# Optimization experiments

Hardware: AMD Instinct MI355X
Metric: run time of the kernel (lower is better)

The kernel has to match this reference:

```python
import jax, jax.numpy as jnp
import numpy as np

N = 100_000   # number of sparse points
C = 128       # channels
K3 = 27       # 3x3x3 kernel offsets


def sparse_conv(x, nbr, W, b):
    """Minkowski-style sparse conv: gather-GEMM-scatter.
    x:   [N, Cin] point features
    nbr: [N, K3] neighbor index per kernel offset; index N -> missing (zero row)
    W:   [K3, Cin, Cout], b: [Cout]
    """
    x_pad = jnp.concatenate([x, jnp.zeros((1, x.shape[1]), x.dtype)], axis=0)

    def step(acc, wk_nk):
        Wk, nk = wk_nk                      # Wk: [Cin,Cout], nk: [N]
        return acc + x_pad[nk] @ Wk, None   # gather + GEMM, accumulate

    acc0 = jnp.broadcast_to(b, (x.shape[0], W.shape[2])).astype(x.dtype)
    acc, _ = jax.lax.scan(step, acc0, (W, nbr.T))
    return acc


def setup_inputs() -> dict:
    key = jax.random.key(0)
    ks = jax.random.split(key, 12)
    Ch = C // 2

    def w(k, shape, fan_in):
        return jax.random.normal(k, shape, dtype=jnp.float32) / np.sqrt(fan_in)

    x = jax.random.normal(ks[0], (N, C), dtype=jnp.float32)
    # neighbor map; value N means "no neighbor" (maps to zero-padded row)
    nbr = jax.random.randint(ks[1], (N, K3), 0, N + 1, dtype=jnp.int32)

    return {
        "x": x,
        "nbr": nbr,
        "W00": w(ks[2], (K3, C, Ch), K3 * C),   # conv0_0: kxkxk, C -> C/2
        "b00": jnp.zeros((Ch,), jnp.float32),
        "W01": w(ks[3], (K3, Ch, Ch), K3 * Ch),  # conv0_1: kxkxk, C/2 -> C/2
        "b01": jnp.zeros((Ch,), jnp.float32),
        "W10": w(ks[4], (C, Ch), C),             # conv1_0: 1x1x1, C -> C/2
        "b10": jnp.zeros((Ch,), jnp.float32),
        "W11": w(ks[5], (K3, Ch, Ch), K3 * Ch),  # conv1_1: kxkxk, C/2 -> C/2
        "b11": jnp.zeros((Ch,), jnp.float32),
        "W12": w(ks[6], (Ch, Ch), Ch),           # conv1_2: 1x1x1, C/2 -> C/2
        "b12": jnp.zeros((Ch,), jnp.float32),
    }


def reference(x, nbr, W00, b00, W01, b01, W10, b10, W11, b11, W12, b12):
    # branch 0: conv -> relu -> conv
    h0 = jax.nn.relu(sparse_conv(x, nbr, W00, b00))
    out0 = sparse_conv(h0, nbr, W01, b01)
    # branch 1: 1x1 conv -> relu -> conv -> relu -> 1x1 conv
    h1 = jax.nn.relu(x @ W10 + b10)
    h1 = jax.nn.relu(sparse_conv(h1, nbr, W11, b11))
    out1 = h1 @ W12 + b12
    # concat channels, residual add
    return jnp.concatenate([out0, out1], axis=1) + x
```

## Files before the change

kernel.cpp:

```cpp
#include <hip/hip_runtime.h>
#include <hip/hip_bf16.h>
#include <stdint.h>

typedef __bf16 bf16x8 __attribute__((ext_vector_type(8)));
typedef float  f32x4  __attribute__((ext_vector_type(4)));

#define MFMA(A, B, C) __builtin_amdgcn_mfma_f32_16x16x32_bf16((A), (B), (C), 0, 0, 0)

#define LDS_BARRIER() asm volatile("s_waitcnt lgkmcnt(0)\n\ts_barrier" ::: "memory")

static __device__ __forceinline__ unsigned short f2b(float f) {
    union { float f; unsigned int u; } v; v.f = f;
    return (unsigned short)((v.u + 0x7FFFu + ((v.u >> 16) & 1u)) >> 16);
}

static __device__ __forceinline__ bf16x8 perm_frag(int sel, bf16x8 D) {
    union { bf16x8 v; int d[4]; } u, r;
    u.v = D;
#pragma unroll
    for (int w = 0; w < 4; ++w) r.d[w] = __builtin_amdgcn_ds_bpermute(sel, u.d[w]);
    return r.v;
}

__global__ __launch_bounds__(256) void convert_kernel(
    const float* __restrict__ x, unsigned short* __restrict__ xb,
    unsigned short* __restrict__ hb, int N) {
    long long i = (long long)blockIdx.x * blockDim.x + threadIdx.x;
    long long base = i * 4;
    long long nx = (long long)N * 128;
    long long total = nx + 128;
    if (base >= total) return;
    if (base < nx) {
        float4 v = *(const float4*)(x + base);
        ushort4 o;
        o.x = f2b(v.x); o.y = f2b(v.y); o.z = f2b(v.z); o.w = f2b(v.w);
        *(ushort4*)(xb + base) = o;
    } else {
        ushort4 z = make_ushort4(0, 0, 0, 0);
        *(ushort4*)(xb + base) = z;
        *(ushort4*)(hb + base) = z;
    }
}

__global__ __launch_bounds__(256) void pack_kernel(
    const float* __restrict__ W00, const float* __restrict__ W01,
    const float* __restrict__ W10, const float* __restrict__ W11,
    const float* __restrict__ W12,
    unsigned short* __restrict__ wp00, unsigned short* __restrict__ wpC,
    unsigned short* __restrict__ wp10, unsigned short* __restrict__ wp12) {
    int g = blockIdx.x * blockDim.x + threadIdx.x;
    const float* W; int cinSteps; int which;
    if (g < 27648)      { W = W00; cinSteps = 4; which = 0; }
    else if (g < 41472) { g -= 27648; W = W01; cinSteps = 2; which = 1; }
    else if (g < 55296) { g -= 41472; W = W11; cinSteps = 2; which = 2; }
    else if (g < 56320) { g -= 55296; W = W10; cinSteps = 4; which = 3; }
    else if (g < 56832) { g -= 56320; W = W12; cinSteps = 2; which = 4; }
    else return;
    int lane = g & 63;
    int st   = g >> 6;
    int t    = st & 3;
    int s    = st >> 2;
    int q = lane >> 4, n16 = lane & 15;
    int k    = s / cinSteps;
    int cinb = (s % cinSteps) * 32;
    int Cin  = cinSteps * 32;
    int cout = t * 16 + n16;
    unsigned short o[8];
#pragma unroll
    for (int j = 0; j < 8; ++j) {
        float v = W[(size_t)(k * Cin + cinb + q * 8 + j) * 64 + cout];
        o[j] = f2b(v);
    }
    unsigned short* dst;
    if (which == 0)      dst = wp00 + (size_t)g * 8;
    else if (which == 1) dst = wpC + (size_t)k * 8192 +
                               ((size_t)(((s & 1) * 4 + t) * 64 + lane)) * 8;
    else if (which == 2) dst = wpC + (size_t)k * 8192 + 4096 +
                               ((size_t)(((s & 1) * 4 + t) * 64 + lane)) * 8;
    else if (which == 3) dst = wp10 + (size_t)g * 8;
    else                 dst = wp12 + (size_t)g * 8;
    *(ushort4*)(dst)     = make_ushort4(o[0], o[1], o[2], o[3]);
    *(ushort4*)(dst + 4) = make_ushort4(o[4], o[5], o[6], o[7]);
}

__global__ __launch_bounds__(256, 2) void passB_kernel(
    const unsigned short* __restrict__ xb, const int* __restrict__ nbr,
    const unsigned short* __restrict__ wp00, const unsigned short* __restrict__ wp10,
    const float* __restrict__ b00, const float* __restrict__ b10,
    unsigned short* __restrict__ hb, int N, int* __restrict__ ctr, int nstrips) {
    __shared__ __align__(16) unsigned short bbuf[2][8192];
    __shared__ int lds_idx[128 * 27];
    __shared__ int sstrip;
    int tid = threadIdx.x;
    int lane = tid & 63;
    int wv   = tid >> 6;
    int q = lane >> 4, n16 = lane & 15;
    int rowq = lane >> 2, chunk = lane & 3;
    int sel = (n16 * 4 + q) * 4;

    for (;;) {
        if (tid == 0) sstrip = atomicAdd(ctr, 1);
        __syncthreads();
        int strip = sstrip;
        if (strip >= nstrips) break;
        int rowbase = strip * 128 + wv * 32;

        int4 br[4];
#pragma unroll
        for (int j = 0; j < 4; ++j) br[j] = *(const int4*)(wp00 + j * 2048 + tid * 8);
        {
            long long gbase = (long long)strip * 128 * 27;
            long long lim = (long long)N * 27 - 1;
            for (int i = tid; i < 3456; i += 256) {
                long long gi = gbase + i; if (gi > lim) gi = lim;
                lds_idx[i] = nbr[gi];
            }
        }
#pragma unroll
        for (int j = 0; j < 4; ++j) *(int4*)(&bbuf[0][j * 2048 + tid * 8]) = br[j];
        __syncthreads();

        f32x4 acc0[2][4];
        f32x4 acc1[2][4];
#pragma unroll
        for (int rs = 0; rs < 2; ++rs)
#pragma unroll
            for (int t = 0; t < 4; ++t) { acc0[rs][t] = (f32x4)0.f; acc1[rs][t] = (f32x4)0.f; }

        int idxb0 = (wv * 32 + rowq) * 27;
        int idxb1 = (wv * 32 + 16 + rowq) * 27;
        int own0 = min(rowbase + rowq, N - 1);
        int own1 = min(rowbase + 16 + rowq, N - 1);

        int ia = lds_idx[idxb0], ib = lds_idx[idxb1];
        bf16x8 D0[4], D1[4];
        {
            const unsigned short* p0 = xb + (size_t)ia * 128 + chunk * 8;
            const unsigned short* p1 = xb + (size_t)ib * 128 + chunk * 8;
#pragma unroll
            for (int s2 = 0; s2 < 4; ++s2) {
                D0[s2] = *(const bf16x8*)(p0 + s2 * 32);
                D1[s2] = *(const bf16x8*)(p1 + s2 * 32);
            }
        }

        for (int k = 0; k < 27; ++k) {
            int buf = k & 1;
            if (k < 26) {
                const unsigned short* src = wp00 + (size_t)(k + 1) * 8192;
#pragma unroll
                for (int j = 0; j < 4; ++j) br[j] = *(const int4*)(src + j * 2048 + tid * 8);
            }
            int ian = (k + 1 < 27) ? lds_idx[idxb0 + k + 1] : own0;
            int ibn = (k + 1 < 27) ? lds_idx[idxb1 + k + 1] : own1;
            bf16x8 D0n[4], D1n[4];
            {
                const unsigned short* p0 = xb + (size_t)ian * 128 + chunk * 8;
                const unsigned short* p1 = xb + (size_t)ibn * 128 + chunk * 8;
#pragma unroll
                for (int s2 = 0; s2 < 4; ++s2) {
                    D0n[s2] = *(const bf16x8*)(p0 + s2 * 32);
                    D1n[s2] = *(const bf16x8*)(p1 + s2 * 32);
                }
            }
            const unsigned short* lb = &bbuf[buf][0];
#pragma unroll
            for (int s2 = 0; s2 < 4; ++s2) {
                bf16x8 A0 = perm_frag(sel, D0[s2]);
                bf16x8 A1 = perm_frag(sel, D1[s2]);
#pragma unroll
                for (int t = 0; t < 4; ++t) {
                    bf16x8 B = *(const bf16x8*)(lb + (s2 * 4 + t) * 512 + lane * 8);
                    acc0[0][t] = MFMA(A0, B, acc0[0][t]);
                    acc0[1][t] = MFMA(A1, B, acc0[1][t]);
                }
            }
            if (k < 26) {
#pragma unroll
                for (int j = 0; j < 4; ++j)
                    *(int4*)(&bbuf[buf ^ 1][j * 2048 + tid * 8]) = br[j];
            }
#pragma unroll
            for (int s2 = 0; s2 < 4; ++s2) { D0[s2] = D0n[s2]; D1[s2] = D1n[s2]; }
            LDS_BARRIER();
        }

#pragma unroll
        for (int s2 = 0; s2 < 4; ++s2) {
            bf16x8 A0 = perm_frag(sel, D0[s2]);
            bf16x8 A1 = perm_frag(sel, D1[s2]);
#pragma unroll
            for (int t = 0; t < 4; ++t) {
                bf16x8 B = *(const bf16x8*)(wp10 + s2 * 2048 + t * 512 + lane * 8);
                acc1[0][t] = MFMA(A0, B, acc1[0][t]);
                acc1[1][t] = MFMA(A1, B, acc1[1][t]);
            }
        }

#pragma unroll
        for (int rs = 0; rs < 2; ++rs)
#pragma unroll
            for (int t = 0; t < 4; ++t) {
                int col = t * 16 + n16;
                float bb0 = b00[col], bb1 = b10[col];
#pragma unroll
                for (int r = 0; r < 4; ++r) {
                    int row = rowbase + rs * 16 + q * 4 + r;
                    if (row < N) {
                        hb[(size_t)row * 128 + col]      = f2b(fmaxf(acc0[rs][t][r] + bb0, 0.f));
                        hb[(size_t)row * 128 + 64 + col] = f2b(fmaxf(acc1[rs][t][r] + bb1, 0.f));
                    }
                }
            }
        __syncthreads();
    }
}

__global__ __launch_bounds__(256, 2) void passC_kernel(
    const unsigned short* __restrict__ hb, const int* __restrict__ nbr,
    const float* __restrict__ x,
    const unsigned short* __restrict__ wpC, const unsigned short* __restrict__ wp12,
    const float* __restrict__ b01, const float* __restrict__ b11,
    const float* __restrict__ b12, float* __restrict__ out, int N,
    int* __restrict__ ctr, int nstrips) {
    __shared__ __align__(16) unsigned short bbuf[2][8192];
    __shared__ int lds_idx[128 * 27];
    __shared__ int sstrip;
    int tid = threadIdx.x;
    int lane = tid & 63;
    int wv   = tid >> 6;
    int q = lane >> 4, n16 = lane & 15;
    int rowq = lane >> 2, chunk = lane & 3;
    int sel = (n16 * 4 + q) * 4;

    for (;;) {
        if (tid == 0) sstrip = atomicAdd(ctr, 1);
        __syncthreads();
        int strip = sstrip;
        if (strip >= nstrips) break;
        int rowbase = strip * 128 + wv * 32;

        int4 br[4];
#pragma unroll
        for (int j = 0; j < 4; ++j) br[j] = *(const int4*)(wpC + j * 2048 + tid * 8);
        {
            long long gbase = (long long)strip * 128 * 27;
            long long lim = (long long)N * 27 - 1;
            for (int i = tid; i < 3456; i += 256) {
                long long gi = gbase + i; if (gi > lim) gi = lim;
                lds_idx[i] = nbr[gi];
            }
        }
#pragma unroll
        for (int j = 0; j < 4; ++j) *(int4*)(&bbuf[0][j * 2048 + tid * 8]) = br[j];
        __syncthreads();

        f32x4 accO0[2][4];
        f32x4 accT[2][4];
#pragma unroll
        for (int rs = 0; rs < 2; ++rs)
#pragma unroll
            for (int t = 0; t < 4; ++t) { accO0[rs][t] = (f32x4)0.f; accT[rs][t] = (f32x4)0.f; }

        int idxb0 = (wv * 32 + rowq) * 27;
        int idxb1 = (wv * 32 + 16 + rowq) * 27;

        int ia = lds_idx[idxb0], ib = lds_idx[idxb1];
        bf16x8 DA0[2], DC0[2], DA1[2], DC1[2];
        {
            const unsigned short* p0 = hb + (size_t)ia * 128 + chunk * 8;
            const unsigned short* p1 = hb + (size_t)ib * 128 + chunk * 8;
#pragma unroll
            for (int s2 = 0; s2 < 2; ++s2) {
                DA0[s2] = *(const bf16x8*)(p0 + s2 * 32);
                DC0[s2] = *(const bf16x8*)(p0 + 64 + s2 * 32);
                DA1[s2] = *(const bf16x8*)(p1 + s2 * 32);
                DC1[s2] = *(const bf16x8*)(p1 + 64 + s2 * 32);
            }
        }

        for (int k = 0; k < 27; ++k) {
            int buf = k & 1;
            if (k < 26) {
                const unsigned short* src = wpC + (size_t)(k + 1) * 8192;
#pragma unroll
                for (int j = 0; j < 4; ++j) br[j] = *(const int4*)(src + j * 2048 + tid * 8);
            }
            bf16x8 DA0n[2], DC0n[2], DA1n[2], DC1n[2];
            if (k < 26) {
                int ian = lds_idx[idxb0 + k + 1];
                int ibn = lds_idx[idxb1 + k + 1];
                const unsigned short* p0 = hb + (size_t)ian * 128 + chunk * 8;
                const unsigned short* p1 = hb + (size_t)ibn * 128 + chunk * 8;
#pragma unroll
                for (int s2 = 0; s2 < 2; ++s2) {
                    DA0n[s2] = *(const bf16x8*)(p0 + s2 * 32);
                    DC0n[s2] = *(const bf16x8*)(p0 + 64 + s2 * 32);
                    DA1n[s2] = *(const bf16x8*)(p1 + s2 * 32);
                    DC1n[s2] = *(const bf16x8*)(p1 + 64 + s2 * 32);
                }
            }
            const unsigned short* lb = &bbuf[buf][0];
#pragma unroll
            for (int s2 = 0; s2 < 2; ++s2) {
                bf16x8 A0 = perm_frag(sel, DA0[s2]);
                bf16x8 A1 = perm_frag(sel, DA1[s2]);
#pragma unroll
                for (int t = 0; t < 4; ++t) {
                    bf16x8 B = *(const bf16x8*)(lb + (s2 * 4 + t) * 512 + lane * 8);
                    accO0[0][t] = MFMA(A0, B, accO0[0][t]);
                    accO0[1][t] = MFMA(A1, B, accO0[1][t]);
                }
                bf16x8 C0 = perm_frag(sel, DC0[s2]);
                bf16x8 C1 = perm_frag(sel, DC1[s2]);
#pragma unroll
                for (int t = 0; t < 4; ++t) {
                    bf16x8 B2 = *(const bf16x8*)(lb + 4096 + (s2 * 4 + t) * 512 + lane * 8);
                    accT[0][t] = MFMA(C0, B2, accT[0][t]);
                    accT[1][t] = MFMA(C1, B2, accT[1][t]);
                }
            }
            if (k < 26) {
#pragma unroll
                for (int j = 0; j < 4; ++j)
                    *(int4*)(&bbuf[buf ^ 1][j * 2048 + tid * 8]) = br[j];
#pragma unroll
                for (int s2 = 0; s2 < 2; ++s2) {
                    DA0[s2] = DA0n[s2]; DC0[s2] = DC0n[s2];
                    DA1[s2] = DA1n[s2]; DC1[s2] = DC1n[s2];
                }
            }
            LDS_BARRIER();
        }

        unsigned short* scratch = &bbuf[0][0];
        unsigned short* myl = scratch + wv * 2304;
#pragma unroll
        for (int rs = 0; rs < 2; ++rs)
#pragma unroll
            for (int t = 0; t < 4; ++t) {
                int col = t * 16 + n16;
                float bo = b01[col], bt = b11[col];
#pragma unroll
                for (int r = 0; r < 4; ++r) {
                    int row = rowbase + rs * 16 + q * 4 + r;
                    if (row < N) {
                        float xv = __builtin_nontemporal_load(x + (size_t)row * 128 + col);
                        __builtin_nontemporal_store(accO0[rs][t][r] + bo + xv,
                                                    out + (size_t)row * 128 + col);
                    }
                    float tv = fmaxf(accT[rs][t][r] + bt, 0.f);
                    myl[(rs * 16 + q * 4 + r) * 72 + col] = f2b(tv);
                }
            }

        f32x4 accO1[2][4];
#pragma unroll
        for (int rs = 0; rs < 2; ++rs)
#pragma unroll
            for (int t = 0; t < 4; ++t) accO1[rs][t] = (f32x4)0.f;
#pragma unroll
        for (int s2 = 0; s2 < 2; ++s2) {
            bf16x8 A0 = *(const bf16x8*)(myl + n16 * 72 + s2 * 32 + q * 8);
            bf16x8 A1 = *(const bf16x8*)(myl + (16 + n16) * 72 + s2 * 32 + q * 8);
#pragma unroll
            for (int t = 0; t < 4; ++t) {
                bf16x8 B = *(const bf16x8*)(wp12 + s2 * 2048 + t * 512 + lane * 8);
                accO1[0][t] = MFMA(A0, B, accO1[0][t]);
                accO1[1][t] = MFMA(A1, B, accO1[1][t]);
            }
        }
#pragma unroll
        for (int rs = 0; rs < 2; ++rs)
#pragma unroll
            for (int t = 0; t < 4; ++t) {
                int col = t * 16 + n16;
                float bo = b12[col];
#pragma unroll
                for (int r = 0; r < 4; ++r) {
                    int row = rowbase + rs * 16 + q * 4 + r;
                    if (row < N) {
                        float xv = __builtin_nontemporal_load(x + (size_t)row * 128 + 64 + col);
                        __builtin_nontemporal_store(accO1[rs][t][r] + bo + xv,
                                                    out + (size_t)row * 128 + 64 + col);
                    }
                }
            }
        __syncthreads();
    }
}

extern "C" void kernel_launch(void* const* d_in, const int* in_sizes, int n_in,
                              void* d_out, int out_size, void* d_ws, size_t ws_size,
                              hipStream_t stream) {
    const float* x   = (const float*)d_in[0];
    const int*   nbr = (const int*)d_in[1];
    const float* W00 = (const float*)d_in[2];
    const float* b00 = (const float*)d_in[3];
    const float* W01 = (const float*)d_in[4];
    const float* b01 = (const float*)d_in[5];
    const float* W10 = (const float*)d_in[6];
    const float* b10 = (const float*)d_in[7];
    const float* W11 = (const float*)d_in[8];
    const float* b11 = (const float*)d_in[9];
    const float* W12 = (const float*)d_in[10];
    const float* b12 = (const float*)d_in[11];
    float* out = (float*)d_out;
    int N = in_sizes[0] / 128;

    char* ws = (char*)d_ws;
    size_t cur = 0;
    unsigned short* xb  = (unsigned short*)(ws + cur); cur += (size_t)(N + 1) * 128 * 2;
    unsigned short* hb  = (unsigned short*)(ws + cur); cur += (size_t)(N + 1) * 128 * 2;
    unsigned short* wp00 = (unsigned short*)(ws + cur); cur += 27648 * 8 * 2;
    unsigned short* wpC  = (unsigned short*)(ws + cur); cur += (size_t)27 * 8192 * 2;
    unsigned short* wp10 = (unsigned short*)(ws + cur); cur += 8192 * 2;
    unsigned short* wp12 = (unsigned short*)(ws + cur); cur += 4096 * 2;
    cur = (cur + 255) & ~(size_t)255;
    int* ctrs = (int*)(ws + cur); cur += 256;

    hipMemsetAsync(ctrs, 0, 8, stream);
    long long cvt_groups = ((long long)N * 128 + 128) / 4;
    int cvt_blocks = (int)((cvt_groups + 255) / 256);
    convert_kernel<<<cvt_blocks, 256, 0, stream>>>(x, xb, hb, N);
    pack_kernel<<<222, 256, 0, stream>>>(W00, W01, W10, W11, W12,
                                         wp00, wpC, wp10, wp12);
    int nstrips = (N + 127) / 128;
    passB_kernel<<<768, 256, 0, stream>>>(xb, nbr, wp00, wp10, b00, b10, hb, N,
                                          ctrs + 0, nstrips);
    passC_kernel<<<768, 256, 0, stream>>>(hb, nbr, x, wpC, wp12,
                                          b01, b11, b12, out, N,
                                          ctrs + 1, nstrips);
}
```

Baseline: 414.4 us.

## Drop LDS weight staging and persistent scheduler; read weights per wave from global

Both conv passes stop double-buffering each kernel offset's weight slab through LDS behind per-iteration block barriers. Each wave now reads B fragments straight from global (L1/L2-resident) memory and uses its own private index slice, so no block-level synchronisation is needed. The atomic-counter persistent strip scheduler and its memset are replaced by one block per 128-row strip, and launch bounds are raised to 3 blocks per SIMD. The cost is more global and L2 traffic for the weights plus higher register pressure from the tighter occupancy bound.

```diff
diff --git a/kernel.cpp b/kernel.cpp
--- a/kernel.cpp
+++ b/kernel.cpp
@@ -6,8 +6,6 @@
 typedef float  f32x4  __attribute__((ext_vector_type(4)));
 
 #define MFMA(A, B, C) __builtin_amdgcn_mfma_f32_16x16x32_bf16((A), (B), (C), 0, 0, 0)
-
-#define LDS_BARRIER() asm volatile("s_waitcnt lgkmcnt(0)\n\ts_barrier" ::: "memory")
 
 static __device__ __forceinline__ unsigned short f2b(float f) {
     union { float f; unsigned int u; } v; v.f = f;
@@ -83,311 +81,262 @@
     *(ushort4*)(dst + 4) = make_ushort4(o[4], o[5], o[6], o[7]);
 }
 
-__global__ __launch_bounds__(256, 2) void passB_kernel(
+__global__ __launch_bounds__(256, 3) void passB_kernel(
     const unsigned short* __restrict__ xb, const int* __restrict__ nbr,
     const unsigned short* __restrict__ wp00, const unsigned short* __restrict__ wp10,
     const float* __restrict__ b00, const float* __restrict__ b10,
-    unsigned short* __restrict__ hb, int N, int* __restrict__ ctr, int nstrips) {
-    __shared__ __align__(16) unsigned short bbuf[2][8192];
-    __shared__ int lds_idx[128 * 27];
-    __shared__ int sstrip;
-    int tid = threadIdx.x;
-    int lane = tid & 63;
-    int wv   = tid >> 6;
-    int q = lane >> 4, n16 = lane & 15;
-    int rowq = lane >> 2, chunk = lane & 3;
-    int sel = (n16 * 4 + q) * 4;
-
-    for (;;) {
-        if (tid == 0) sstrip = atomicAdd(ctr, 1);
-        __syncthreads();
-        int strip = sstrip;
-        if (strip >= nstrips) break;
-        int rowbase = strip * 128 + wv * 32;
-
-        int4 br[4];
-#pragma unroll
-        for (int j = 0; j < 4; ++j) br[j] = *(const int4*)(wp00 + j * 2048 + tid * 8);
+    unsigned short* __restrict__ hb, int N) {
+    __shared__ int lds_idx[4][864];
+    const int tid  = threadIdx.x;
+    const int lane = tid & 63;
+    const int wv   = tid >> 6;
+    const int q = lane >> 4, n16 = lane & 15;
+    const int rowq = lane >> 2, chunk = lane & 3;
+    const int sel = (n16 * 4 + q) * 4;
+
+    int rowbase = blockIdx.x * 128 + wv * 32;
+    if (rowbase >= N) return;
+
+    {
+        long long gbase = (long long)rowbase * 27;
+        long long lim = (long long)N * 27 - 1;
+        int* dst = lds_idx[wv];
+        for (int i = lane; i < 864; i += 64) {
+            long long gi = gbase + i; if (gi > lim) gi = lim;
+            dst[i] = nbr[gi];
+        }
+    }
+
+    f32x4 acc0[2][4];
+    f32x4 acc1[2][4];
+#pragma unroll
+    for (int rs = 0; rs < 2; ++rs)
+#pragma unroll
+        for (int t = 0; t < 4; ++t) { acc0[rs][t] = (f32x4)0.f; acc1[rs][t] = (f32x4)0.f; }
+
+    const int idxb0 = rowq * 27;
+    const int idxb1 = (16 + rowq) * 27;
+    const int own0 = rowbase + rowq;
+    const int own1 = rowbase + 16 + rowq;
+
+    int ia = lds_idx[wv][idxb0], ib = lds_idx[wv][idxb1];
+    bf16x8 D0[4], D1[4];
+    {
+        const unsigned short* p0 = xb + (size_t)ia * 128 + chunk * 8;
+        const unsigned short* p1 = xb + (size_t)ib * 128 + chunk * 8;
+#pragma unroll
+        for (int s2 = 0; s2 < 4; ++s2) {
+            D0[s2] = *(const bf16x8*)(p0 + s2 * 32);
+            D1[s2] = *(const bf16x8*)(p1 + s2 * 32);
+        }
+    }
+
+    for (int k = 0; k < 27; ++k) {
+        int ian = (k + 1 < 27) ? lds_idx[wv][idxb0 + k + 1] : own0;
+        int ibn = (k + 1 < 27) ? lds_idx[wv][idxb1 + k + 1] : own1;
+        bf16x8 D0n[4], D1n[4];
         {
-            long long gbase = (long long)strip * 128 * 27;
-            long long lim = (long long)N * 27 - 1;
-            for (int i = tid; i < 3456; i += 256) {
-                long long gi = gbase + i; if (gi > lim) gi = lim;
-                lds_idx[i] = nbr[gi];
-            }
-        }
-#pragma unroll
-        for (int j = 0; j < 4; ++j) *(int4*)(&bbuf[0][j * 2048 + tid * 8]) = br[j];
-        __syncthreads();
-
-        f32x4 acc0[2][4];
-        f32x4 acc1[2][4];
-#pragma unroll
-        for (int rs = 0; rs < 2; ++rs)
-#pragma unroll
-            for (int t = 0; t < 4; ++t) { acc0[rs][t] = (f32x4)0.f; acc1[rs][t] = (f32x4)0.f; }
-
-        int idxb0 = (wv * 32 + rowq) * 27;
-        int idxb1 = (wv * 32 + 16 + rowq) * 27;
-        int own0 = min(rowbase + rowq, N - 1);
-        int own1 = min(rowbase + 16 + rowq, N - 1);
-
-        int ia = lds_idx[idxb0], ib = lds_idx[idxb1];
-        bf16x8 D0[4], D1[4];
-        {
-            const unsigned short* p0 = xb + (size_t)ia * 128 + chunk * 8;
-            const unsigned short* p1 = xb + (size_t)ib * 128 + chunk * 8;
+            const unsigned short* p0 = xb + (size_t)ian * 128 + chunk * 8;
+            const unsigned short* p1 = xb + (size_t)ibn * 128 + chunk * 8;
 #pragma unroll
             for (int s2 = 0; s2 < 4; ++s2) {
-                D0[s2] = *(const bf16x8*)(p0 + s2 * 32);
-                D1[s2] = *(const bf16x8*)(p1 + s2 * 32);
-            }
-        }
-
-        for (int k = 0; k < 27; ++k) {
-            int buf = k & 1;
-            if (k < 26) {
-                const unsigned short* src = wp00 + (size_t)(k + 1) * 8192;
-#pragma unroll
-                for (int j = 0; j < 4; ++j) br[j] = *(const int4*)(src + j * 2048 + tid * 8);
-            }
-            int ian = (k + 1 < 27) ? lds_idx[idxb0 + k + 1] : own0;
-            int ibn = (k + 1 < 27) ? lds_idx[idxb1 + k + 1] : own1;
-            bf16x8 D0n[4], D1n[4];
-            {
-                const unsigned short* p0 = xb + (size_t)ian * 128 + chunk * 8;
-                const unsigned short* p1 = xb + (size_t)ibn * 128 + chunk * 8;
-#pragma unroll
-                for (int s2 = 0; s2 < 4; ++s2) {
-                    D0n[s2] = *(const bf16x8*)(p0 + s2 * 32);
-                    D1n[s2] = *(const bf16x8*)(p1 + s2 * 32);
-                }
-            }
-            const unsigned short* lb = &bbuf[buf][0];
-#pragma unroll
-            for (int s2 = 0; s2 < 4; ++s2) {
-                bf16x8 A0 = perm_frag(sel, D0[s2]);
-                bf16x8 A1 = perm_frag(sel, D1[s2]);
-#pragma unroll
-                for (int t = 0; t < 4; ++t) {
-                    bf16x8 B = *(const bf16x8*)(lb + (s2 * 4 + t) * 512 + lane * 8);
-                    acc0[0][t] = MFMA(A0, B, acc0[0][t]);
-                    acc0[1][t] = MFMA(A1, B, acc0[1][t]);
-                }
-            }
-            if (k < 26) {
-#pragma unroll
-                for (int j = 0; j < 4; ++j)
-                    *(int4*)(&bbuf[buf ^ 1][j * 2048 + tid * 8]) = br[j];
-            }
-#pragma unroll
-            for (int s2 = 0; s2 < 4; ++s2) { D0[s2] = D0n[s2]; D1[s2] = D1n[s2]; }
-            LDS_BARRIER();
-        }
-
+                D0n[s2] = *(const bf16x8*)(p0 + s2 * 32);
+                D1n[s2] = *(const bf16x8*)(p1 + s2 * 32);
+            }
+        }
+        const unsigned short* wb = wp00 + (size_t)k * 8192;
 #pragma unroll
         for (int s2 = 0; s2 < 4; ++s2) {
             bf16x8 A0 = perm_frag(sel, D0[s2]);
             bf16x8 A1 = perm_frag(sel, D1[s2]);
 #pragma unroll
             for (int t = 0; t < 4; ++t) {
-                bf16x8 B = *(const bf16x8*)(wp10 + s2 * 2048 + t * 512 + lane * 8);
-                acc1[0][t] = MFMA(A0, B, acc1[0][t]);
-                acc1[1][t] = MFMA(A1, B, acc1[1][t]);
-            }
-        }
-
-#pragma unroll
-        for (int rs = 0; rs < 2; ++rs)
-#pragma unroll
-            for (int t = 0; t < 4; ++t) {
-                int col = t * 16 + n16;
-                float bb0 = b00[col], bb1 = b10[col];
-#pragma unroll
-                for (int r = 0; r < 4; ++r) {
-                    int row = rowbase + rs * 16 + q * 4 + r;
-                    if (row < N) {
-                        hb[(size_t)row * 128 + col]      = f2b(fmaxf(acc0[rs][t][r] + bb0, 0.f));
-                        hb[(size_t)row * 128 + 64 + col] = f2b(fmaxf(acc1[rs][t][r] + bb1, 0.f));
-                    }
+                bf16x8 B = *(const bf16x8*)(wb + (s2 * 4 + t) * 512 + lane * 8);
+                acc0[0][t] = MFMA(A0, B, acc0[0][t]);
+                acc0[1][t] = MFMA(A1, B, acc0[1][t]);
+            }
+        }
+#pragma unroll
+        for (int s2 = 0; s2 < 4; ++s2) { D0[s2] = D0n[s2]; D1[s2] = D1n[s2]; }
+    }
+
+#pragma unroll
+    for (int s2 = 0; s2 < 4; ++s2) {
+        bf16x8 A0 = perm_frag(sel, D0[s2]);
+        bf16x8 A1 = perm_frag(sel, D1[s2]);
+#pragma unroll
+        for (int t = 0; t < 4; ++t) {
+            bf16x8 B = *(const bf16x8*)(wp10 + s2 * 2048 + t * 512 + lane * 8);
+            acc1[0][t] = MFMA(A0, B, acc1[0][t]);
+            acc1[1][t] = MFMA(A1, B, acc1[1][t]);
+        }
+    }
+
+#pragma unroll
+    for (int rs = 0; rs < 2; ++rs)
+#pragma unroll
+        for (int t = 0; t < 4; ++t) {
+            int col = t * 16 + n16;
+            float bb0 = b00[col], bb1 = b10[col];
+#pragma unroll
+            for (int r = 0; r < 4; ++r) {
+                int row = rowbase + rs * 16 + q * 4 + r;
+                if (row < N) {
+                    hb[(size_t)row * 128 + col]      = f2b(fmaxf(acc0[rs][t][r] + bb0, 0.f));
+                    hb[(size_t)row * 128 + 64 + col] = f2b(fmaxf(acc1[rs][t][r] + bb1, 0.f));
                 }
             }
-        __syncthreads();
-    }
-}
-
-__global__ __launch_bounds__(256, 2) void passC_kernel(
+        }
+}
+
+__global__ __launch_bounds__(256, 3) void passC_kernel(
     const unsigned short* __restrict__ hb, const int* __restrict__ nbr,
     const float* __restrict__ x,
     const unsigned short* __restrict__ wpC, const unsigned short* __restrict__ wp12,
     const float* __restrict__ b01, const float* __restrict__ b11,
-    const float* __restrict__ b12, float* __restrict__ out, int N,
-    int* __restrict__ ctr, int nstrips) {
-    __shared__ __align__(16) unsigned short bbuf[2][8192];
-    __shared__ int lds_idx[128 * 27];
-    __shared__ int sstrip;
-    int tid = threadIdx.x;
-    int lane = tid & 63;
-    int wv   = tid >> 6;
-    int q = lane >> 4, n16 = lane & 15;
-    int rowq = lane >> 2, chunk = lane & 3;
-    int sel = (n16 * 4 + q) * 4;
-
-    for (;;) {
-        if (tid == 0) sstrip = atomicAdd(ctr, 1);
-        __syncthreads();
-        int strip = sstrip;
-        if (strip >= nstrips) break;
-        int rowbase = strip * 128 + wv * 32;
-
-        int4 br[4];
-#pragma unroll
-        for (int j = 0; j < 4; ++j) br[j] = *(const int4*)(wpC + j * 2048 + tid * 8);
-        {
-            long long gbase = (long long)strip * 128 * 27;
-            long long lim = (long long)N * 27 - 1;
-            for (int i = tid; i < 3456; i += 256) {
-                long long gi = gbase + i; if (gi > lim) gi = lim;
-                lds_idx[i] = nbr[gi];
-            }
-        }
-#pragma unroll
-        for (int j = 0; j < 4; ++j) *(int4*)(&bbuf[0][j * 2048 + tid * 8]) = br[j];
-        __syncthreads();
-
-        f32x4 accO0[2][4];
-        f32x4 accT[2][4];
-#pragma unroll
-        for (int rs = 0; rs < 2; ++rs)
-#pragma unroll
-            for (int t = 0; t < 4; ++t) { accO0[rs][t] = (f32x4)0.f; accT[rs][t] = (f32x4)0.f; }
-
-        int idxb0 = (wv * 32 + rowq) * 27;
-        int idxb1 = (wv * 32 + 16 + rowq) * 27;
-
-        int ia = lds_idx[idxb0], ib = lds_idx[idxb1];
-        bf16x8 DA0[2], DC0[2], DA1[2], DC1[2];
-        {
-            const unsigned short* p0 = hb + (size_t)ia * 128 + chunk * 8;
-            const unsigned short* p1 = hb + (size_t)ib * 128 + chunk * 8;
+    const float* __restrict__ b12, float* __restrict__ out, int N) {
+    __shared__ int lds_idx[4][864];
+    __shared__ __align__(16) unsigned short scr[4][2304];
+    const int tid  = threadIdx.x;
+    const int lane = tid & 63;
+    const int wv   = tid >> 6;
+    const int q = lane >> 4, n16 = lane & 15;
+    const int rowq = lane >> 2, chunk = lane & 3;
+    const int sel = (n16 * 4 + q) * 4;
+
+    int rowbase = blockIdx.x * 128 + wv * 32;
+    if (rowbase >= N) return;
+
+    {
+        long long gbase = (long long)rowbase * 27;
+        long long lim = (long long)N * 27 - 1;
+        int* dst = lds_idx[wv];
+        for (int i = lane; i < 864; i += 64) {
+            long long gi = gbase + i; if (gi > lim) gi = lim;
+            dst[i] = nbr[gi];
+        }
+    }
+
+    f32x4 accO0[2][4];
+    f32x4 accT[2][4];
+#pragma unroll
+    for (int rs = 0; rs < 2; ++rs)
+#pragma unroll
+        for (int t = 0; t < 4; ++t) { accO0[rs][t] = (f32x4)0.f; accT[rs][t] = (f32x4)0.f; }
+
+    const int idxb0 = rowq * 27;
+    const int idxb1 = (16 + rowq) * 27;
+
+    int ia = lds_idx[wv][idxb0], ib = lds_idx[wv][idxb1];
+    bf16x8 DA0[2], DC0[2], DA1[2], DC1[2];
+    {
+        const unsigned short* p0 = hb + (size_t)ia * 128 + chunk * 8;
+        const unsigned short* p1 = hb + (size_t)ib * 128 + chunk * 8;
+#pragma unroll
+        for (int s2 = 0; s2 < 2; ++s2) {
+            DA0[s2] = *(const bf16x8*)(p0 + s2 * 32);
+            DC0[s2] = *(const bf16x8*)(p0 + 64 + s2 * 32);
+            DA1[s2] = *(const bf16x8*)(p1 + s2 * 32);
+            DC1[s2] = *(const bf16x8*)(p1 + 64 + s2 * 32);
+        }
+    }
+
+    for (int k = 0; k < 27; ++k) {
+        bf16x8 DA0n[2], DC0n[2], DA1n[2], DC1n[2];
+        if (k < 26) {
+            int ian = lds_idx[wv][idxb0 + k + 1];
+            int ibn = lds_idx[wv][idxb1 + k + 1];
+            const unsigned short* p0 = hb + (size_t)ian * 128 + chunk * 8;
+            const unsigned short* p1 = hb + (size_t)ibn * 128 + chunk * 8;
 #pragma unroll
             for (int s2 = 0; s2 < 2; ++s2) {
-                DA0[s2] = *(const bf16x8*)(p0 + s2 * 32);
-                DC0[s2] = *(const bf16x8*)(p0 + 64 + s2 * 32);
-                DA1[s2] = *(const bf16x8*)(p1 + s2 * 32);
-                DC1[s2] = *(const bf16x8*)(p1 + 64 + s2 * 32);
-            }
-        }
-
-        for (int k = 0; k < 27; ++k) {
-            int buf = k & 1;
-            if (k < 26) {
-                const unsigned short* src = wpC + (size_t)(k + 1) * 8192;
-#pragma unroll
-                for (int j = 0; j < 4; ++j) br[j] = *(const int4*)(src + j * 2048 + tid * 8);
-            }
-            bf16x8 DA0n[2], DC0n[2], DA1n[2], DC1n[2];
-            if (k < 26) {
-                int ian = lds_idx[idxb0 + k + 1];
-                int ibn = lds_idx[idxb1 + k + 1];
-                const unsigned short* p0 = hb + (size_t)ian * 128 + chunk * 8;
-                const unsigned short* p1 = hb + (size_t)ibn * 128 + chunk * 8;
-#pragma unroll
-                for (int s2 = 0; s2 < 2; ++s2) {
-                    DA0n[s2] = *(const bf16x8*)(p0 + s2 * 32);
-                    DC0n[s2] = *(const bf16x8*)(p0 + 64 + s2 * 32);
-                    DA1n[s2] = *(const bf16x8*)(p1 + s2 * 32);
-                    DC1n[s2] = *(const bf16x8*)(p1 + 64 + s2 * 32);
+                DA0n[s2] = *(const bf16x8*)(p0 + s2 * 32);
+                DC0n[s2] = *(const bf16x8*)(p0 + 64 + s2 * 32);
+                DA1n[s2] = *(const bf16x8*)(p1 + s2 * 32);
+                DC1n[s2] = *(const bf16x8*)(p1 + 64 + s2 * 32);
+            }
+        }
+        const unsigned short* wb = wpC + (size_t)k * 8192;
+#pragma unroll
+        for (int s2 = 0; s2 < 2; ++s2) {
+            bf16x8 A0 = perm_frag(sel, DA0[s2]);
+            bf16x8 A1 = perm_frag(sel, DA1[s2]);
+#pragma unroll
+            for (int t = 0; t < 4; ++t) {
+                bf16x8 B = *(const bf16x8*)(wb + (s2 * 4 + t) * 512 + lane * 8);
+                accO0[0][t] = MFMA(A0, B, accO0[0][t]);
+                accO0[1][t] = MFMA(A1, B, accO0[1][t]);
+            }
+            bf16x8 C0 = perm_frag(sel, DC0[s2]);
+            bf16x8 C1 = perm_frag(sel, DC1[s2]);
+#pragma unroll
+            for (int t = 0; t < 4; ++t) {
+                bf16x8 B2 = *(const bf16x8*)(wb + 4096 + (s2 * 4 + t) * 512 + lane * 8);
+                accT[0][t] = MFMA(C0, B2, accT[0][t]);
+                accT[1][t] = MFMA(C1, B2, accT[1][t]);
+            }
+        }
+        if (k < 26) {
+#pragma unroll
+            for (int s2 = 0; s2 < 2; ++s2) {
+                DA0[s2] = DA0n[s2]; DC0[s2] = DC0n[s2];
+                DA1[s2] = DA1n[s2]; DC1[s2] = DC1n[s2];
+            }
+        }
+    }
+
+    unsigned short* myl = scr[wv];
+#pragma unroll
+    for (int rs = 0; rs < 2; ++rs)
+#pragma unroll
+        for (int t = 0; t < 4; ++t) {
+            int col = t * 16 + n16;
+            float bo = b01[col], bt = b11[col];
+#pragma unroll
+            for (int r = 0; r < 4; ++r) {
+                int row = rowbase + rs * 16 + q * 4 + r;
+                if (row < N) {
+                    float xv = __builtin_nontemporal_load(x + (size_t)row * 128 + col);
+                    __builtin_nontemporal_store(accO0[rs][t][r] + bo + xv,
+                                                out + (size_t)row * 128 + col);
                 }
-            }
-            const unsigned short* lb = &bbuf[buf][0];
-#pragma unroll
-            for (int s2 = 0; s2 < 2; ++s2) {
-                bf16x8 A0 = perm_frag(sel, DA0[s2]);
-                bf16x8 A1 = perm_frag(sel, DA1[s2]);
-#pragma unroll
-                for (int t = 0; t < 4; ++t) {
-                    bf16x8 B = *(const bf16x8*)(lb + (s2 * 4 + t) * 512 + lane * 8);
-                    accO0[0][t] = MFMA(A0, B, accO0[0][t]);
-                    accO0[1][t] = MFMA(A1, B, accO0[1][t]);
+                float tv = fmaxf(accT[rs][t][r] + bt, 0.f);
+                myl[(rs * 16 + q * 4 + r) * 72 + col] = f2b(tv);
+            }
+        }
+
+    f32x4 accO1[2][4];
+#pragma unroll
+    for (int rs = 0; rs < 2; ++rs)
+#pragma unroll
+        for (int t = 0; t < 4; ++t) accO1[rs][t] = (f32x4)0.f;
+#pragma unroll
+    for (int s2 = 0; s2 < 2; ++s2) {
+        bf16x8 A0 = *(const bf16x8*)(myl + n16 * 72 + s2 * 32 + q * 8);
+        bf16x8 A1 = *(const bf16x8*)(myl + (16 + n16) * 72 + s2 * 32 + q * 8);
+#pragma unroll
+        for (int t = 0; t < 4; ++t) {
+            bf16x8 B = *(const bf16x8*)(wp12 + s2 * 2048 + t * 512 + lane * 8);
+            accO1[0][t] = MFMA(A0, B, accO1[0][t]);
+            accO1[1][t] = MFMA(A1, B, accO1[1][t]);
+        }
+    }
+#pragma unroll
+    for (int rs = 0; rs < 2; ++rs)
+#pragma unroll
+        for (int t = 0; t < 4; ++t) {
+            int col = t * 16 + n16;
+            float bo = b12[col];
+#pragma unroll
+            for (int r = 0; r < 4; ++r) {
+                int row = rowbase + rs * 16 + q * 4 + r;
+                if (row < N) {
+                    float xv = __builtin_nontemporal_load(x + (size_t)row * 128 + 64 + col);
+                    __builtin_nontemporal_store(accO1[rs][t][r] + bo + xv,
+                                                out + (size_t)row * 128 + 64 + col);
                 }
-                bf16x8 C0 = perm_frag(sel, DC0[s2]);
-                bf16x8 C1 = perm_frag(sel, DC1[s2]);
-#pragma unroll
-                for (int t = 0; t < 4; ++t) {
-                    bf16x8 B2 = *(const bf16x8*)(lb + 4096 + (s2 * 4 + t) * 512 + lane * 8);
-                    accT[0][t] = MFMA(C0, B2, accT[0][t]);
-                    accT[1][t] = MFMA(C1, B2, accT[1][t]);
-                }
-            }
-            if (k < 26) {
-#pragma unroll
-                for (int j = 0; j < 4; ++j)
-                    *(int4*)(&bbuf[buf ^ 1][j * 2048 + tid * 8]) = br[j];
-#pragma unroll
-                for (int s2 = 0; s2 < 2; ++s2) {
-                    DA0[s2] = DA0n[s2]; DC0[s2] = DC0n[s2];
-                    DA1[s2] = DA1n[s2]; DC1[s2] = DC1n[s2];
-                }
-            }
-            LDS_BARRIER();
-        }
-
-        unsigned short* scratch = &bbuf[0][0];
-        unsigned short* myl = scratch + wv * 2304;
-#pragma unroll
-        for (int rs = 0; rs < 2; ++rs)
-#pragma unroll
-            for (int t = 0; t < 4; ++t) {
-                int col = t * 16 + n16;
-                float bo = b01[col], bt = b11[col];
-#pragma unroll
-                for (int r = 0; r < 4; ++r) {
-                    int row = rowbase + rs * 16 + q * 4 + r;
-                    if (row < N) {
-                        float xv = __builtin_nontemporal_load(x + (size_t)row * 128 + col);
-                        __builtin_nontemporal_store(accO0[rs][t][r] + bo + xv,
-                                                    out + (size_t)row * 128 + col);
-                    }
-                    float tv = fmaxf(accT[rs][t][r] + bt, 0.f);
-                    myl[(rs * 16 + q * 4 + r) * 72 + col] = f2b(tv);
-                }
-            }
-
-        f32x4 accO1[2][4];
-#pragma unroll
-        for (int rs = 0; rs < 2; ++rs)
-#pragma unroll
-            for (int t = 0; t < 4; ++t) accO1[rs][t] = (f32x4)0.f;
-#pragma unroll
-        for (int s2 = 0; s2 < 2; ++s2) {
-            bf16x8 A0 = *(const bf16x8*)(myl + n16 * 72 + s2 * 32 + q * 8);
-            bf16x8 A1 = *(const bf16x8*)(myl + (16 + n16) * 72 + s2 * 32 + q * 8);
-#pragma unroll
-            for (int t = 0; t < 4; ++t) {
-                bf16x8 B = *(const bf16x8*)(wp12 + s2 * 2048 + t * 512 + lane * 8);
-                accO1[0][t] = MFMA(A0, B, accO1[0][t]);
-                accO1[1][t] = MFMA(A1, B, accO1[1][t]);
-            }
-        }
-#pragma unroll
-        for (int rs = 0; rs < 2; ++rs)
-#pragma unroll
-            for (int t = 0; t < 4; ++t) {
-                int col = t * 16 + n16;
-                float bo = b12[col];
-#pragma unroll
-                for (int r = 0; r < 4; ++r) {
-                    int row = rowbase + rs * 16 + q * 4 + r;
-                    if (row < N) {
-                        float xv = __builtin_nontemporal_load(x + (size_t)row * 128 + 64 + col);
-                        __builtin_nontemporal_store(accO1[rs][t][r] + bo + xv,
-                                                    out + (size_t)row * 128 + 64 + col);
-                    }
-                }
-            }
-        __syncthreads();
-    }
+            }
+        }
 }
 
 extern "C" void kernel_launch(void* const* d_in, const int* in_sizes, int n_in,
@@ -416,19 +365,14 @@
     unsigned short* wpC  = (unsigned short*)(ws + cur); cur += (size_t)27 * 8192 * 2;
     unsigned short* wp10 = (unsigned short*)(ws + cur); cur += 8192 * 2;
     unsigned short* wp12 = (unsigned short*)(ws + cur); cur += 4096 * 2;
-    cur = (cur + 255) & ~(size_t)255;
-    int* ctrs = (int*)(ws + cur); cur += 256;
-
-    hipMemsetAsync(ctrs, 0, 8, stream);
+
     long long cvt_groups = ((long long)N * 128 + 128) / 4;
     int cvt_blocks = (int)((cvt_groups + 255) / 256);
     convert_kernel<<<cvt_blocks, 256, 0, stream>>>(x, xb, hb, N);
     pack_kernel<<<222, 256, 0, stream>>>(W00, W01, W10, W11, W12,
                                          wp00, wpC, wp10, wp12);
     int nstrips = (N + 127) / 128;
-    passB_kernel<<<768, 256, 0, stream>>>(xb, nbr, wp00, wp10, b00, b10, hb, N,
-                                          ctrs + 0, nstrips);
-    passC_kernel<<<768, 256, 0, stream>>>(hb, nbr, x, wpC, wp12,
-                                          b01, b11, b12, out, N,
-                                          ctrs + 1, nstrips);
-}
+    passB_kernel<<<nstrips, 256, 0, stream>>>(xb, nbr, wp00, wp10, b00, b10, hb, N);
+    passC_kernel<<<nstrips, 256, 0, stream>>>(hb, nbr, x, wpC, wp12,
+                                              b01, b11, b12, out, N);
+}
```

Measured after the change: 471.6 us. +13.8%, slower.
